# Performance work log

Measured on AMD Instinct MI355X. Metric: run time of the kernel, lower is better.

The kernel has to match this reference:

```python
import jax, jax.numpy as jnp
import numpy as np

DIM = 768
DIM_QKV = 64
NUM_HEAD = 12
EPS = 1e-5


def layer_norm(x, gamma, beta):
    mu = jnp.mean(x, axis=-1, keepdims=True)
    var = jnp.mean(jnp.square(x - mu), axis=-1, keepdims=True)
    return (x - mu) * jax.lax.rsqrt(var + EPS) * gamma + beta


def setup_inputs() -> dict:
    key = jax.random.key(0)
    ks = jax.random.split(key, 10)
    s = 0.02
    x = jax.random.normal(ks[0], (4, 2048, DIM), dtype=jnp.float32)
    wq = jax.random.normal(ks[1], (DIM, DIM_QKV), dtype=jnp.float32) * s
    wk = jax.random.normal(ks[2], (DIM, DIM_QKV), dtype=jnp.float32) * s
    wv = jax.random.normal(ks[3], (DIM, DIM_QKV), dtype=jnp.float32) * s
    lin_w = jax.random.normal(ks[4], (DIM_QKV * NUM_HEAD, DIM), dtype=jnp.float32) * s
    lin_b = jnp.zeros((DIM,), dtype=jnp.float32)
    ln1_g = jnp.ones((DIM,), dtype=jnp.float32)
    ln1_b = jnp.zeros((DIM,), dtype=jnp.float32)
    fc1_w = jax.random.normal(ks[5], (DIM, 4 * DIM), dtype=jnp.float32) * s
    fc1_b = jnp.zeros((4 * DIM,), dtype=jnp.float32)
    fc2_w = jax.random.normal(ks[6], (4 * DIM, DIM), dtype=jnp.float32) * s
    fc2_b = jnp.zeros((DIM,), dtype=jnp.float32)
    return {"x": x, "wq": wq, "wk": wk, "wv": wv, "lin_w": lin_w,
            "lin_b": lin_b, "ln1_g": ln1_g, "ln1_b": ln1_b,
            "fc1_w": fc1_w, "fc1_b": fc1_b, "fc2_w": fc2_w, "fc2_b": fc2_b}


def reference(x, wq, wk, wv, lin_w, lin_b, ln1_g, ln1_b, fc1_w, fc1_b, fc2_w, fc2_b):
    identity1 = x
    h = layer_norm(x, ln1_g, ln1_b)
    # single shared-weight attention head (original calls the same module num_head times)
    q = h @ wq  # [B,S,Dq]
    k = h @ wk
    v = h @ wv
    scores = jnp.einsum('bik,bjk->bij', q, k) / (DIM_QKV ** 0.5)  # [B,S,S]
    attn = jax.nn.softmax(scores, axis=-1)
    out_head = attn @ v  # [B,S,Dq]
    # concat of num_head identical outputs == tile along last dim
    cat = jnp.tile(out_head, (1, 1, NUM_HEAD))  # [B,S,Dq*H]
    attn_out = cat @ lin_w + lin_b
    out = attn_out + identity1
    identity2 = out
    # NOTE: original reuses layer_norm_1 here (layer_norm_2 is unused)
    out = layer_norm(out, ln1_g, ln1_b)
    out = jax.nn.gelu(out @ fc1_w + fc1_b, approximate=False)
    out = out @ fc2_w + fc2_b
    return out + identity2
```

## Files before the change

### kernel.cpp

```cpp
#include <hip/hip_runtime.h>

typedef unsigned short u16;
typedef unsigned int u32;
typedef __bf16 bf16x8 __attribute__((ext_vector_type(8)));
typedef float f32x4 __attribute__((ext_vector_type(4)));

__device__ __forceinline__ u16 f2bf(float f) {
  u32 u = __float_as_uint(f);
  u32 r = (u + 0x7FFFu + ((u >> 16) & 1u)) >> 16;
  return (u16)r;
}

__device__ __forceinline__ float gelu_exact(float x) {
  return 0.5f * x * (1.f + erff(x * 0.70710678118654752f));
}

__device__ __forceinline__ void gload16(const u16* g, u16* l) {
  __builtin_amdgcn_global_load_lds((const __attribute__((address_space(1))) void*)g,
                                   (__attribute__((address_space(3))) void*)l, 16, 0, 0);
}

__global__ void transpose_cast(const float* __restrict__ in, u16* __restrict__ out,
                               int R, int C) {
  __shared__ float tile[32][33];
  int c0 = blockIdx.x * 32, r0 = blockIdx.y * 32;
  int tx = threadIdx.x, ty = threadIdx.y;
  for (int i = 0; i < 32; i += 8) {
    int r = r0 + ty + i, c = c0 + tx;
    tile[ty + i][tx] = (r < R && c < C) ? in[(long)r * C + c] : 0.f;
  }
  __syncthreads();
  for (int i = 0; i < 32; i += 8) {
    int oc = c0 + ty + i, orr = r0 + tx;
    if (oc < C && orr < R) out[(long)oc * R + orr] = f2bf(tile[tx][ty + i]);
  }
}

__global__ void weff_build(const float* __restrict__ lin_w, u16* __restrict__ weffT) {
  int idx = blockIdx.x * 256 + threadIdx.x;
  if (idx >= 768 * 64) return;
  int n = idx % 768, d = idx / 768;
  float s = 0.f;
#pragma unroll
  for (int j = 0; j < 12; j++) s += lin_w[(long)(j * 64 + d) * 768 + n];
  weffT[(long)n * 64 + d] = f2bf(s);
}

__global__ __launch_bounds__(256)
void ln_rows(const float* __restrict__ in, const float* __restrict__ gamma,
             const float* __restrict__ beta, u16* __restrict__ out, int nrows) {
  int gid = blockIdx.x * blockDim.x + threadIdx.x;
  int wid = gid >> 6, l = gid & 63;
  if (wid >= nrows) return;
  const float4* row = (const float4*)(in + (long)wid * 768);
  float4 v[3];
  float s = 0.f, s2 = 0.f;
#pragma unroll
  for (int j = 0; j < 3; j++) {
    v[j] = row[l + 64 * j];
    s += v[j].x + v[j].y + v[j].z + v[j].w;
    s2 += v[j].x * v[j].x + v[j].y * v[j].y + v[j].z * v[j].z + v[j].w * v[j].w;
  }
#pragma unroll
  for (int off = 1; off < 64; off <<= 1) {
    s += __shfl_xor(s, off);
    s2 += __shfl_xor(s2, off);
  }
  float mean = s * (1.f / 768.f);
  float rstd = rsqrtf(s2 * (1.f / 768.f) - mean * mean + 1e-5f);
  u16* orow = out + (long)wid * 768;
#pragma unroll
  for (int j = 0; j < 3; j++) {
    float4 g = ((const float4*)gamma)[l + 64 * j];
    float4 b = ((const float4*)beta)[l + 64 * j];
    ushort4 o;
    o.x = f2bf((v[j].x - mean) * rstd * g.x + b.x);
    o.y = f2bf((v[j].y - mean) * rstd * g.y + b.y);
    o.z = f2bf((v[j].z - mean) * rstd * g.z + b.z);
    o.w = f2bf((v[j].w - mean) * rstd * g.w + b.w);
    ((ushort4*)orow)[l + 64 * j] = o;
  }
}

template <int EPI>
__global__ __launch_bounds__(256, 2)
void gemm_bt(const u16* __restrict__ A, const u16* __restrict__ Bt,
             const float* __restrict__ bias, const float* __restrict__ res,
             void* __restrict__ outv, int M, int N, int K, int ldo) {
  __shared__ __align__(16) u16 Alds[128 * 32];
  __shared__ __align__(16) u16 Blds[128 * 32];
  const int t = threadIdx.x;
  const int w = t >> 6, l = t & 63;
  const int wr = w >> 1, wc = w & 1;
  const int srow = w * 32 + (l >> 2);
  const int scol = (l & 3) * 8;
  const u16* aptr = A + (long)(blockIdx.x * 128 + srow) * K + scol;
  const u16* bptr = Bt + (long)(blockIdx.y * 128 + srow) * K + scol;
  const long j16 = (long)16 * K;
  u16* albase = &Alds[(w * 32) * 32];
  u16* blbase = &Blds[(w * 32) * 32];
  const int ar = (wr * 64 + (l & 15)) * 32 + (l >> 4) * 8;
  const int br = (wc * 64 + (l & 15)) * 32 + (l >> 4) * 8;
  f32x4 acc[4][4] = {};
  for (int ks = 0; ks < K; ks += 32) {
    __syncthreads();
    gload16(aptr, albase);
    gload16(aptr + j16, albase + 16 * 32);
    gload16(bptr, blbase);
    gload16(bptr + j16, blbase + 16 * 32);
    asm volatile("s_waitcnt vmcnt(0)" ::: "memory");
    __syncthreads();
    bf16x8 af[4], bfr[4];
#pragma unroll
    for (int i = 0; i < 4; i++) af[i] = *(const bf16x8*)(&Alds[ar + i * 16 * 32]);
#pragma unroll
    for (int i = 0; i < 4; i++) bfr[i] = *(const bf16x8*)(&Blds[br + i * 16 * 32]);
#pragma unroll
    for (int mf = 0; mf < 4; mf++)
#pragma unroll
      for (int nf = 0; nf < 4; nf++)
        acc[mf][nf] = __builtin_amdgcn_mfma_f32_16x16x32_bf16(af[mf], bfr[nf], acc[mf][nf], 0, 0, 0);
    aptr += 32;
    bptr += 32;
  }
  const int rowbase = blockIdx.x * 128 + wr * 64 + ((l >> 4) * 4);
  const int colbase = blockIdx.y * 128 + wc * 64 + (l & 15);
#pragma unroll
  for (int nf = 0; nf < 4; nf++) {
    int col = colbase + nf * 16;
    if (col >= N) continue;
    float bv = (EPI == 0) ? 0.f : bias[col];
#pragma unroll
    for (int mf = 0; mf < 4; mf++) {
#pragma unroll
      for (int i = 0; i < 4; i++) {
        long row = rowbase + mf * 16 + i;
        float v = acc[mf][nf][i] + bv;
        if (EPI == 2) v = gelu_exact(v);
        if (EPI == 1) {
          v += res[row * ldo + col];
          ((float*)outv)[row * ldo + col] = v;
        } else {
          ((u16*)outv)[row * ldo + col] = f2bf(v);
        }
      }
    }
  }
}

__global__ __launch_bounds__(128)
void attn_fwd(const u16* __restrict__ qkv, float* __restrict__ pout,
              float* __restrict__ pm, float* __restrict__ pl) {
  __shared__ __align__(16) u16 Klds[32 * 72];
  __shared__ __align__(16) u16 Vlds[64 * 40];
  __shared__ __align__(16) u16 Plds[2][16 * 40];
  const int t = threadIdx.x, w = t >> 6, l = t & 63;
  const int r0 = blockIdx.x * 32;
  const int sp = blockIdx.y;
  const long bb = (long)(r0 & ~2047);
  const int qrow = r0 + w * 16 + (l & 15);
  bf16x8 qf0 = *(const bf16x8*)(qkv + (long)qrow * 192 + ((l >> 4) * 8));
  bf16x8 qf1 = *(const bf16x8*)(qkv + (long)qrow * 192 + 32 + ((l >> 4) * 8));
  f32x4 po[4] = {};
  float m_i[4], l_i[4];
#pragma unroll
  for (int i = 0; i < 4; i++) { m_i[i] = -1e30f; l_i[i] = 0.f; }
  const int kkey = t >> 3, kseg = t & 7;
  for (int st = sp * 512; st < sp * 512 + 512; st += 32) {
    uint4 k0 = *(const uint4*)(qkv + (bb + st + kkey) * 192 + 64 + kseg * 8);
    uint4 k1 = *(const uint4*)(qkv + (bb + st + 16 + kkey) * 192 + 64 + kseg * 8);
    u16 vv[16];
#pragma unroll
    for (int i = 0; i < 16; i++) {
      int e = t + 128 * i;
      vv[i] = qkv[(bb + st + (e >> 6)) * 192 + 128 + (e & 63)];
    }
    __syncthreads();
    *(uint4*)(&Klds[kkey * 72 + kseg * 8]) = k0;
    *(uint4*)(&Klds[(16 + kkey) * 72 + kseg * 8]) = k1;
#pragma unroll
    for (int i = 0; i < 16; i++) {
      int e = t + 128 * i;
      Vlds[(e & 63) * 40 + (e >> 6)] = vv[i];
    }
    __syncthreads();
    f32x4 s0 = {}, s1 = {};
    {
      bf16x8 ka = *(const bf16x8*)(&Klds[(l & 15) * 72 + ((l >> 4) * 8)]);
      bf16x8 kb = *(const bf16x8*)(&Klds[(l & 15) * 72 + 32 + ((l >> 4) * 8)]);
      s0 = __builtin_amdgcn_mfma_f32_16x16x32_bf16(qf0, ka, s0, 0, 0, 0);
      s0 = __builtin_amdgcn_mfma_f32_16x16x32_bf16(qf1, kb, s0, 0, 0, 0);
      bf16x8 kc = *(const bf16x8*)(&Klds[(16 + (l & 15)) * 72 + ((l >> 4) * 8)]);
      bf16x8 kd = *(const bf16x8*)(&Klds[(16 + (l & 15)) * 72 + 32 + ((l >> 4) * 8)]);
      s1 = __builtin_amdgcn_mfma_f32_16x16x32_bf16(qf0, kc, s1, 0, 0, 0);
      s1 = __builtin_amdgcn_mfma_f32_16x16x32_bf16(qf1, kd, s1, 0, 0, 0);
    }
    float sf[4];
#pragma unroll
    for (int i = 0; i < 4; i++) {
      float a = s0[i] * 0.125f, b = s1[i] * 0.125f;
      float tm = fmaxf(a, b);
#pragma unroll
      for (int off = 1; off < 16; off <<= 1) tm = fmaxf(tm, __shfl_xor(tm, off));
      float mn = fmaxf(m_i[i], tm);
      sf[i] = __expf(m_i[i] - mn);
      m_i[i] = mn;
      a = __expf(a - mn);
      b = __expf(b - mn);
      float rs = a + b;
#pragma unroll
      for (int off = 1; off < 16; off <<= 1) rs += __shfl_xor(rs, off);
      l_i[i] = l_i[i] * sf[i] + rs;
      int prow = (l >> 4) * 4 + i;
      Plds[w][prow * 40 + (l & 15)] = f2bf(a);
      Plds[w][prow * 40 + 16 + (l & 15)] = f2bf(b);
    }
#pragma unroll
    for (int n = 0; n < 4; n++)
#pragma unroll
      for (int i = 0; i < 4; i++) po[n][i] *= sf[i];
    bf16x8 pf = *(const bf16x8*)(&Plds[w][(l & 15) * 40 + ((l >> 4) * 8)]);
#pragma unroll
    for (int n = 0; n < 4; n++) {
      bf16x8 vf = *(const bf16x8*)(&Vlds[(n * 16 + (l & 15)) * 40 + ((l >> 4) * 8)]);
      po[n] = __builtin_amdgcn_mfma_f32_16x16x32_bf16(pf, vf, po[n], 0, 0, 0);
    }
  }
#pragma unroll
  for (int i = 0; i < 4; i++) {
    long row = r0 + w * 16 + ((l >> 4) * 4) + i;
    if ((l & 15) == 0) {
      pm[(long)sp * 8192 + row] = m_i[i];
      pl[(long)sp * 8192 + row] = l_i[i];
    }
#pragma unroll
    for (int n = 0; n < 4; n++)
      pout[((long)sp * 8192 + row) * 64 + n * 16 + (l & 15)] = po[n][i];
  }
}

__global__ __launch_bounds__(256)
void attn_merge(const float* __restrict__ pout, const float* __restrict__ pm,
                const float* __restrict__ pl, u16* __restrict__ oh) {
  int gid = blockIdx.x * 256 + threadIdx.x;
  int row = gid >> 6;
  float M = -1e30f;
#pragma unroll
  for (int s = 0; s < 4; s++) M = fmaxf(M, pm[s * 8192 + row]);
  float L = 0.f, acc = 0.f;
#pragma unroll
  for (int s = 0; s < 4; s++) {
    float e = __expf(pm[s * 8192 + row] - M);
    L += pl[s * 8192 + row] * e;
    acc += pout[((long)s * 8192 + row) * 64 + (gid & 63)] * e;
  }
  oh[gid] = f2bf(acc / L);
}

extern "C" void kernel_launch(void* const* d_in, const int* in_sizes, int n_in,
                              void* d_out, int out_size, void* d_ws, size_t ws_size,
                              hipStream_t stream) {
  const float* x = (const float*)d_in[0];
  const float* wq = (const float*)d_in[1];
  const float* wk = (const float*)d_in[2];
  const float* wv = (const float*)d_in[3];
  const float* lin_w = (const float*)d_in[4];
  const float* lin_b = (const float*)d_in[5];
  const float* ln1_g = (const float*)d_in[6];
  const float* ln1_b = (const float*)d_in[7];
  const float* fc1_w = (const float*)d_in[8];
  const float* fc1_b = (const float*)d_in[9];
  const float* fc2_w = (const float*)d_in[10];
  const float* fc2_b = (const float*)d_in[11];
  float* out = (float*)d_out;

  char* p = (char*)d_ws;
  u16* wqkvT = (u16*)p; p += 256 * 768 * 2;
  u16* weffT = (u16*)p; p += 768 * 64 * 2;
  u16* fc1wT = (u16*)p; p += (size_t)3072 * 768 * 2;
  u16* fc2wT = (u16*)p; p += (size_t)768 * 3072 * 2;
  u16* h = (u16*)p; p += (size_t)8192 * 768 * 2;
  u16* qkv = (u16*)p; p += (size_t)8192 * 192 * 2;
  u16* oh = (u16*)p; p += (size_t)8192 * 64 * 2;
  float* out1 = (float*)p; p += (size_t)8192 * 768 * 4;
  u16* a1 = (u16*)p; p += (size_t)8192 * 3072 * 2;
  float* pout = (float*)a1;
  float* pm = pout + (size_t)4 * 8192 * 64;
  float* pl = pm + 4 * 8192;

  dim3 tb(32, 8);
  transpose_cast<<<dim3(2, 24), tb, 0, stream>>>(wq, wqkvT, 768, 64);
  transpose_cast<<<dim3(2, 24), tb, 0, stream>>>(wk, wqkvT + 64 * 768, 768, 64);
  transpose_cast<<<dim3(2, 24), tb, 0, stream>>>(wv, wqkvT + 128 * 768, 768, 64);
  hipMemsetAsync(wqkvT + 192 * 768, 0, 64 * 768 * 2, stream);
  transpose_cast<<<dim3(96, 24), tb, 0, stream>>>(fc1_w, fc1wT, 768, 3072);
  transpose_cast<<<dim3(24, 96), tb, 0, stream>>>(fc2_w, fc2wT, 3072, 768);
  weff_build<<<192, 256, 0, stream>>>(lin_w, weffT);

  ln_rows<<<2048, 256, 0, stream>>>(x, ln1_g, ln1_b, h, 8192);
  gemm_bt<0><<<dim3(64, 2), 256, 0, stream>>>(h, wqkvT, nullptr, nullptr, qkv,
                                              8192, 192, 768, 192);
  attn_fwd<<<dim3(256, 4), 128, 0, stream>>>(qkv, pout, pm, pl);
  attn_merge<<<2048, 256, 0, stream>>>(pout, pm, pl, oh);
  gemm_bt<1><<<dim3(64, 6), 256, 0, stream>>>(oh, weffT, lin_b, x, out1,
                                              8192, 768, 64, 768);
  ln_rows<<<2048, 256, 0, stream>>>(out1, ln1_g, ln1_b, h, 8192);
  gemm_bt<2><<<dim3(64, 24), 256, 0, stream>>>(h, fc1wT, fc1_b, nullptr, a1,
                                               8192, 3072, 768, 3072);
  gemm_bt<1><<<dim3(64, 6), 256, 0, stream>>>(a1, fc2wT, fc2_b, out1, out,
                                              8192, 768, 3072, 768);
}
```

Before: 332.8 us.

## Use 256x256 8-wave pipelined GEMM for FC1/FC2 with split-K FC2 reduce

Replaces the 128x128 gemm_bt for the two MLP GEMMs with a new 512-thread kernel that uses 256x256 tiles, swizzled LDS staging via global_load_lds, double buffering and interleaved MFMA phases with priority hints. FC2 is split along K into two bf16 partial outputs, which a separate elementwise kernel sums together with bias and residual. The goal is higher MFMA utilisation and better reuse on the large GEMMs and more blocks for FC2. The cost is an extra partial-sum buffer and kernel, and rounding the FC2 partials to bf16 before summation loses some precision. The GELU line removed from gemm_bt only affects its FC1 instantiation, which is no longer used.

```diff
diff --git a/kernel.cpp b/kernel.cpp
--- a/kernel.cpp
+++ b/kernel.cpp
@@ -4,11 +4,15 @@
 typedef unsigned int u32;
 typedef __bf16 bf16x8 __attribute__((ext_vector_type(8)));
 typedef float f32x4 __attribute__((ext_vector_type(4)));
+typedef u16 ushortx8 __attribute__((ext_vector_type(8)));
 
 __device__ __forceinline__ u16 f2bf(float f) {
   u32 u = __float_as_uint(f);
   u32 r = (u + 0x7FFFu + ((u >> 16) & 1u)) >> 16;
   return (u16)r;
+}
+__device__ __forceinline__ float bf2f(u16 v) {
+  return __uint_as_float((u32)v << 16);
 }
 
 __device__ __forceinline__ float gelu_exact(float x) {
@@ -136,7 +140,6 @@
       for (int i = 0; i < 4; i++) {
         long row = rowbase + mf * 16 + i;
         float v = acc[mf][nf][i] + bv;
-        if (EPI == 2) v = gelu_exact(v);
         if (EPI == 1) {
           v += res[row * ldo + col];
           ((float*)outv)[row * ldo + col] = v;
@@ -146,6 +149,137 @@
       }
     }
   }
+}
+
+template <int EPI>
+__global__ __launch_bounds__(512, 2)
+void gemm8p(const u16* __restrict__ A, const u16* __restrict__ Bt,
+            const float* __restrict__ bias, u16* __restrict__ outv,
+            int M, int N, int lda, int Ks, int ldo) {
+  __shared__ __align__(16) u16 lds[2][2][16384];
+  const int t = threadIdx.x;
+  const int w = t >> 6, l = t & 63;
+  const int wm = w >> 2, wn = w & 3;
+  const int NT = Ks >> 6;
+  const long kb = (long)blockIdx.z * Ks;
+  const u16* Ag = A + (long)blockIdx.x * 256 * lda + kb;
+  const u16* Bg = Bt + (long)blockIdx.y * 256 * lda + kb;
+  const int c0 = t, c1 = t + 512;
+  const int r0 = c0 >> 3, r1 = c1 >> 3;
+  const int co0 = ((c0 & 7) ^ (r0 & 7)) << 3;
+  const int co1 = ((c1 & 7) ^ (r1 & 7)) << 3;
+  const int db0 = w * 512;
+  const int db1 = 4096 + w * 512;
+  const int arb = (wm * 128 + (l & 15)) * 64;
+  const int brb = (wn * 64 + (l & 15)) * 64;
+  const int ck0 = (((l >> 4) + 0) ^ (l & 7)) << 3;
+  const int ck1 = (((l >> 4) + 4) ^ (l & 7)) << 3;
+
+  f32x4 acc[8][4] = {};
+  bf16x8 a[4][2], b0[2][2], b1[2][2];
+
+  auto STAGE = [&](int s) {
+    if (s >= 4 * NT) return;
+    int T = s >> 2, h = s & 3;
+    int isB = (h == 0 || h == 3);
+    int half = h >> 1;
+    u16* base = &lds[T & 1][isB][half * 8192];
+    const u16* src = (isB ? Bg : Ag) + (long)(half * 128) * lda + T * 64;
+    gload16(src + (long)r0 * lda + co0, base + db0);
+    gload16(src + (long)r1 * lda + co1, base + db1);
+  };
+  auto LDA_ = [&](int buf, int qm) {
+#pragma unroll
+    for (int i = 0; i < 4; i++) {
+      const u16* base = &lds[buf][0][arb + (qm * 4 + i) * 1024];
+      a[i][0] = *(const bf16x8*)(base + ck0);
+      a[i][1] = *(const bf16x8*)(base + ck1);
+    }
+  };
+  auto LDB_ = [&](int buf, int qn, bf16x8 (&bb)[2][2]) {
+#pragma unroll
+    for (int j = 0; j < 2; j++) {
+      const u16* base = &lds[buf][1][brb + (qn * 2 + j) * 1024];
+      bb[j][0] = *(const bf16x8*)(base + ck0);
+      bb[j][1] = *(const bf16x8*)(base + ck1);
+    }
+  };
+  auto MM = [&](int qm, int qn, bf16x8 (&bb)[2][2]) {
+    __builtin_amdgcn_s_setprio(1);
+#pragma unroll
+    for (int i = 0; i < 4; i++)
+#pragma unroll
+      for (int j = 0; j < 2; j++)
+#pragma unroll
+        for (int ks = 0; ks < 2; ks++)
+          acc[qm * 4 + i][qn * 2 + j] = __builtin_amdgcn_mfma_f32_16x16x32_bf16(
+              a[i][ks], bb[j][ks], acc[qm * 4 + i][qn * 2 + j], 0, 0, 0);
+    __builtin_amdgcn_s_setprio(0);
+  };
+  auto SB = [&]() {
+    __builtin_amdgcn_s_barrier();
+    __builtin_amdgcn_sched_barrier(0);
+  };
+
+  for (int i = 0; i < 6; i++) STAGE(i);
+  asm volatile("s_waitcnt vmcnt(4)" ::: "memory");
+  SB();
+  for (int T = 0; T < NT; T++) {
+    const int buf = T & 1;
+    LDA_(buf, 0); LDB_(buf, 0, b0); STAGE(4 * T + 6);
+    SB(); MM(0, 0, b0); SB();
+    LDB_(buf, 1, b1); STAGE(4 * T + 7);
+    SB(); MM(0, 1, b1); SB();
+    LDA_(buf, 1); STAGE(4 * T + 8);
+    SB(); MM(1, 1, b1); SB();
+    STAGE(4 * T + 9);
+    if (T < NT - 2) { asm volatile("s_waitcnt vmcnt(4)" ::: "memory"); }
+    else            { asm volatile("s_waitcnt vmcnt(0)" ::: "memory"); }
+    SB(); MM(1, 0, b0); SB();
+  }
+
+  const int rowb = blockIdx.x * 256 + wm * 128 + ((l >> 4) * 4);
+  const int colb = blockIdx.y * 256 + wn * 64 + (l & 15);
+  u16* op = outv + (EPI == 4 ? (size_t)blockIdx.z * M * ldo : (size_t)0);
+#pragma unroll
+  for (int nf = 0; nf < 4; nf++) {
+    int col = colb + nf * 16;
+    float bv = (EPI == 2) ? bias[col] : 0.f;
+#pragma unroll
+    for (int mf = 0; mf < 8; mf++) {
+#pragma unroll
+      for (int i = 0; i < 4; i++) {
+        long row = rowb + mf * 16 + i;
+        float v = acc[mf][nf][i] + bv;
+        if (EPI == 2) v = gelu_exact(v);
+        op[row * ldo + col] = f2bf(v);
+      }
+    }
+  }
+}
+
+__global__ __launch_bounds__(256)
+void fc2_reduce(const u16* __restrict__ p, const float* __restrict__ bias,
+                const float* __restrict__ res, float* __restrict__ out) {
+  size_t base = ((size_t)blockIdx.x * 256 + threadIdx.x) * 8;
+  ushortx8 pa = *(const ushortx8*)(p + base);
+  ushortx8 pb = *(const ushortx8*)(p + (size_t)8192 * 768 + base);
+  int col = (int)(base % 768);
+  float4 r0 = *(const float4*)(res + base);
+  float4 r1 = *(const float4*)(res + base + 4);
+  float4 g0 = *(const float4*)(bias + col);
+  float4 g1 = *(const float4*)(bias + col + 4);
+  float4 o0, o1;
+  o0.x = bf2f(pa[0]) + bf2f(pb[0]) + r0.x + g0.x;
+  o0.y = bf2f(pa[1]) + bf2f(pb[1]) + r0.y + g0.y;
+  o0.z = bf2f(pa[2]) + bf2f(pb[2]) + r0.z + g0.z;
+  o0.w = bf2f(pa[3]) + bf2f(pb[3]) + r0.w + g0.w;
+  o1.x = bf2f(pa[4]) + bf2f(pb[4]) + r1.x + g1.x;
+  o1.y = bf2f(pa[5]) + bf2f(pb[5]) + r1.y + g1.y;
+  o1.z = bf2f(pa[6]) + bf2f(pb[6]) + r1.z + g1.z;
+  o1.w = bf2f(pa[7]) + bf2f(pb[7]) + r1.w + g1.w;
+  *(float4*)(out + base) = o0;
+  *(float4*)(out + base + 4) = o1;
 }
 
 __global__ __launch_bounds__(128)
@@ -284,6 +418,7 @@
   u16* oh = (u16*)p; p += (size_t)8192 * 64 * 2;
   float* out1 = (float*)p; p += (size_t)8192 * 768 * 4;
   u16* a1 = (u16*)p; p += (size_t)8192 * 3072 * 2;
+  u16* fc2p = (u16*)p; p += (size_t)2 * 8192 * 768 * 2;
   float* pout = (float*)a1;
   float* pm = pout + (size_t)4 * 8192 * 64;
   float* pl = pm + 4 * 8192;
@@ -305,8 +440,9 @@
   gemm_bt<1><<<dim3(64, 6), 256, 0, stream>>>(oh, weffT, lin_b, x, out1,
                                               8192, 768, 64, 768);
   ln_rows<<<2048, 256, 0, stream>>>(out1, ln1_g, ln1_b, h, 8192);
-  gemm_bt<2><<<dim3(64, 24), 256, 0, stream>>>(h, fc1wT, fc1_b, nullptr, a1,
-                                               8192, 3072, 768, 3072);
-  gemm_bt<1><<<dim3(64, 6), 256, 0, stream>>>(a1, fc2wT, fc2_b, out1, out,
-                                              8192, 768, 3072, 768);
-}
+  gemm8p<2><<<dim3(32, 12), 512, 0, stream>>>(h, fc1wT, fc1_b, a1,
+                                              8192, 3072, 768, 768, 3072);
+  gemm8p<4><<<dim3(32, 3, 2), 512, 0, stream>>>(a1, fc2wT, nullptr, fc2p,
+                                                8192, 768, 3072, 1536, 768);
+  fc2_reduce<<<3072, 256, 0, stream>>>(fc2p, fc2_b, out1, out);
+}
```

New measurement: 355.0 us. +6.7%, slower.

## Double-buffer GEMM LDS tiles and split attention keys into eight chunks

Applied to the files above, without the earlier changes.

The bf16 GEMM now keeps two LDS buffers for A and B. It issues the async global-to-LDS loads for the next K step before running the MFMAs on the current one, so there is one barrier per iteration instead of two plus an explicit vmcnt wait. The attention kernel splits each row's keys into eight chunks of 256 instead of four of 512, doubling the grid for more parallelism. The merge kernel and workspace offsets are updated to match. The cost is double the LDS use in the GEMM, more partial-output traffic in the merge, and a reliance on __syncthreads to wait for the async LDS loads.

```diff
diff --git a/kernel.cpp b/kernel.cpp
--- a/kernel.cpp
+++ b/kernel.cpp
@@ -87,8 +87,8 @@
 void gemm_bt(const u16* __restrict__ A, const u16* __restrict__ Bt,
              const float* __restrict__ bias, const float* __restrict__ res,
              void* __restrict__ outv, int M, int N, int K, int ldo) {
-  __shared__ __align__(16) u16 Alds[128 * 32];
-  __shared__ __align__(16) u16 Blds[128 * 32];
+  __shared__ __align__(16) u16 Alds[2][128 * 32];
+  __shared__ __align__(16) u16 Blds[2][128 * 32];
   const int t = threadIdx.x;
   const int w = t >> 6, l = t & 63;
   const int wr = w >> 1, wc = w & 1;
@@ -97,31 +97,40 @@
   const u16* aptr = A + (long)(blockIdx.x * 128 + srow) * K + scol;
   const u16* bptr = Bt + (long)(blockIdx.y * 128 + srow) * K + scol;
   const long j16 = (long)16 * K;
-  u16* albase = &Alds[(w * 32) * 32];
-  u16* blbase = &Blds[(w * 32) * 32];
+  const int lw = (w * 32) * 32;
   const int ar = (wr * 64 + (l & 15)) * 32 + (l >> 4) * 8;
   const int br = (wc * 64 + (l & 15)) * 32 + (l >> 4) * 8;
   f32x4 acc[4][4] = {};
-  for (int ks = 0; ks < K; ks += 32) {
-    __syncthreads();
-    gload16(aptr, albase);
-    gload16(aptr + j16, albase + 16 * 32);
-    gload16(bptr, blbase);
-    gload16(bptr + j16, blbase + 16 * 32);
-    asm volatile("s_waitcnt vmcnt(0)" ::: "memory");
-    __syncthreads();
+  const int ksteps = K >> 5;
+  gload16(aptr, &Alds[0][lw]);
+  gload16(aptr + j16, &Alds[0][lw + 16 * 32]);
+  gload16(bptr, &Blds[0][lw]);
+  gload16(bptr + j16, &Blds[0][lw + 16 * 32]);
+  aptr += 32;
+  bptr += 32;
+  __syncthreads();
+  for (int ks = 0; ks < ksteps; ks++) {
+    const int cur = ks & 1;
+    if (ks + 1 < ksteps) {
+      const int nxt = cur ^ 1;
+      gload16(aptr, &Alds[nxt][lw]);
+      gload16(aptr + j16, &Alds[nxt][lw + 16 * 32]);
+      gload16(bptr, &Blds[nxt][lw]);
+      gload16(bptr + j16, &Blds[nxt][lw + 16 * 32]);
+      aptr += 32;
+      bptr += 32;
+    }
     bf16x8 af[4], bfr[4];
 #pragma unroll
-    for (int i = 0; i < 4; i++) af[i] = *(const bf16x8*)(&Alds[ar + i * 16 * 32]);
-#pragma unroll
-    for (int i = 0; i < 4; i++) bfr[i] = *(const bf16x8*)(&Blds[br + i * 16 * 32]);
+    for (int i = 0; i < 4; i++) af[i] = *(const bf16x8*)(&Alds[cur][ar + i * 16 * 32]);
+#pragma unroll
+    for (int i = 0; i < 4; i++) bfr[i] = *(const bf16x8*)(&Blds[cur][br + i * 16 * 32]);
 #pragma unroll
     for (int mf = 0; mf < 4; mf++)
 #pragma unroll
       for (int nf = 0; nf < 4; nf++)
         acc[mf][nf] = __builtin_amdgcn_mfma_f32_16x16x32_bf16(af[mf], bfr[nf], acc[mf][nf], 0, 0, 0);
-    aptr += 32;
-    bptr += 32;
+    __syncthreads();
   }
   const int rowbase = blockIdx.x * 128 + wr * 64 + ((l >> 4) * 4);
   const int colbase = blockIdx.y * 128 + wc * 64 + (l & 15);
@@ -166,7 +175,7 @@
 #pragma unroll
   for (int i = 0; i < 4; i++) { m_i[i] = -1e30f; l_i[i] = 0.f; }
   const int kkey = t >> 3, kseg = t & 7;
-  for (int st = sp * 512; st < sp * 512 + 512; st += 32) {
+  for (int st = sp * 256; st < sp * 256 + 256; st += 32) {
     uint4 k0 = *(const uint4*)(qkv + (bb + st + kkey) * 192 + 64 + kseg * 8);
     uint4 k1 = *(const uint4*)(qkv + (bb + st + 16 + kkey) * 192 + 64 + kseg * 8);
     u16 vv[16];
@@ -246,10 +255,10 @@
   int row = gid >> 6;
   float M = -1e30f;
 #pragma unroll
-  for (int s = 0; s < 4; s++) M = fmaxf(M, pm[s * 8192 + row]);
+  for (int s = 0; s < 8; s++) M = fmaxf(M, pm[s * 8192 + row]);
   float L = 0.f, acc = 0.f;
 #pragma unroll
-  for (int s = 0; s < 4; s++) {
+  for (int s = 0; s < 8; s++) {
     float e = __expf(pm[s * 8192 + row] - M);
     L += pl[s * 8192 + row] * e;
     acc += pout[((long)s * 8192 + row) * 64 + (gid & 63)] * e;
@@ -285,8 +294,8 @@
   float* out1 = (float*)p; p += (size_t)8192 * 768 * 4;
   u16* a1 = (u16*)p; p += (size_t)8192 * 3072 * 2;
   float* pout = (float*)a1;
-  float* pm = pout + (size_t)4 * 8192 * 64;
-  float* pl = pm + 4 * 8192;
+  float* pm = pout + (size_t)8 * 8192 * 64;
+  float* pl = pm + 8 * 8192;
 
   dim3 tb(32, 8);
   transpose_cast<<<dim3(2, 24), tb, 0, stream>>>(wq, wqkvT, 768, 64);
@@ -300,7 +309,7 @@
   ln_rows<<<2048, 256, 0, stream>>>(x, ln1_g, ln1_b, h, 8192);
   gemm_bt<0><<<dim3(64, 2), 256, 0, stream>>>(h, wqkvT, nullptr, nullptr, qkv,
                                               8192, 192, 768, 192);
-  attn_fwd<<<dim3(256, 4), 128, 0, stream>>>(qkv, pout, pm, pl);
+  attn_fwd<<<dim3(256, 8), 128, 0, stream>>>(qkv, pout, pm, pl);
   attn_merge<<<2048, 256, 0, stream>>>(pout, pm, pl, oh);
   gemm_bt<1><<<dim3(64, 6), 256, 0, stream>>>(oh, weffT, lin_b, x, out1,
                                               8192, 768, 64, 768);
```

Result: slower. 339.9 us (+2.1%).
